# Kernel tuning notes

Measured on AMD Instinct MI355X. Metric: run time of the kernel, lower is better.

Reference implementation:

```python
import jax, jax.numpy as jnp
import numpy as np
from jax import lax

D_MODEL = 1024
D_INNER = 2048   # expand * d_model
D_STATE = 16
D_CONV = 4
DT_RANK = 64     # ceil(d_model / 16)
B_SZ, L_SEQ = 2, 2048


def setup_inputs() -> dict:
    key = jax.random.key(0)
    ks = jax.random.split(key, 12)
    s = lambda *sh: 1.0 / np.sqrt(sh[-1])
    inp = {
        "x": jax.random.normal(ks[0], (B_SZ, L_SEQ, D_MODEL), jnp.float32),
        "in_proj_w": jax.random.normal(ks[1], (2 * D_INNER, D_MODEL), jnp.float32) * s(D_MODEL),
        "conv_w": jax.random.normal(ks[2], (D_INNER, 1, D_CONV), jnp.float32) * 0.3,
        "conv_b": jax.random.normal(ks[3], (D_INNER,), jnp.float32) * 0.05,
        "x_proj_w": jax.random.normal(ks[4], (DT_RANK + 2 * D_STATE, D_INNER), jnp.float32) * s(D_INNER),
        "dt_proj_w": jax.random.normal(ks[5], (D_INNER, DT_RANK), jnp.float32) * s(DT_RANK),
        "dt_proj_b": jnp.log(jnp.exp(jax.random.uniform(ks[6], (D_INNER,), jnp.float32, 1e-3, 1e-1)) - 1.0),
        "A_log": jnp.log(jnp.broadcast_to(jnp.arange(1, D_STATE + 1, dtype=jnp.float32), (D_INNER, D_STATE))),
        "D": jnp.ones((D_INNER,), jnp.float32),
        "out_proj_w": jax.random.normal(ks[7], (D_MODEL, D_INNER), jnp.float32) * s(D_INNER),
        "ln_w": jnp.ones((D_MODEL,), jnp.float32),
        "ln_b": jnp.zeros((D_MODEL,), jnp.float32),
    }
    return inp


def _mamba(x, in_proj_w, conv_w, conv_b, x_proj_w, dt_proj_w, dt_proj_b, A_log, D, out_proj_w):
    # x: [B, L, d_model]
    xz = x @ in_proj_w.T                             # [B, L, 2*d_inner]
    u, z = jnp.split(xz, 2, axis=-1)                 # [B, L, d_inner] each
    # depthwise causal conv1d along L
    u_c = jnp.swapaxes(u, 1, 2)                      # [B, d_inner, L]
    u_c = lax.conv_general_dilated(
        u_c, conv_w, window_strides=(1,), padding=[(D_CONV - 1, 0)],
        feature_group_count=D_INNER, dimension_numbers=("NCH", "OIH", "NCH"))
    u_c = u_c + conv_b[None, :, None]
    u_c = jax.nn.silu(jnp.swapaxes(u_c, 1, 2))       # [B, L, d_inner]
    # input-dependent dt, B, C
    x_dbl = u_c @ x_proj_w.T                         # [B, L, dt_rank + 2*d_state]
    dt_lr = x_dbl[..., :DT_RANK]
    Bm = x_dbl[..., DT_RANK:DT_RANK + D_STATE]       # [B, L, d_state]
    Cm = x_dbl[..., DT_RANK + D_STATE:]              # [B, L, d_state]
    dt = jax.nn.softplus(dt_lr @ dt_proj_w.T + dt_proj_b)  # [B, L, d_inner]
    A = -jnp.exp(A_log)                              # [d_inner, d_state]

    def step(h, inputs):
        dt_t, b_t, c_t, u_t = inputs                 # [B,d_inner],[B,N],[B,N],[B,d_inner]
        dA = jnp.exp(dt_t[:, :, None] * A)           # [B, d_inner, N]
        h = h * dA + (dt_t * u_t)[:, :, None] * b_t[:, None, :]
        y_t = jnp.einsum("bdn,bn->bd", h, c_t)
        return h, y_t

    h0 = jnp.zeros((x.shape[0], D_INNER, D_STATE), x.dtype)
    xs = (jnp.swapaxes(dt, 0, 1), jnp.swapaxes(Bm, 0, 1),
          jnp.swapaxes(Cm, 0, 1), jnp.swapaxes(u_c, 0, 1))
    _, ys = lax.scan(step, h0, xs)                   # ys: [L, B, d_inner]
    y = jnp.swapaxes(ys, 0, 1) + u_c * D             # skip connection D*u
    y = y * jax.nn.silu(z)                           # gate
    return y @ out_proj_w.T                          # [B, L, d_model]


def _layernorm(x, w, b, eps=1e-5):
    mu = jnp.mean(x, axis=-1, keepdims=True)
    var = jnp.mean(jnp.square(x - mu), axis=-1, keepdims=True)
    return (x - mu) * lax.rsqrt(var + eps) * w + b


def reference(x, in_proj_w, conv_w, conv_b, x_proj_w, dt_proj_w, dt_proj_b,
              A_log, D, out_proj_w, ln_w, ln_b):
    y = _mamba(x, in_proj_w, conv_w, conv_b, x_proj_w, dt_proj_w, dt_proj_b,
               A_log, D, out_proj_w)
    return _layernorm(y + x, ln_w, ln_b)  # dropout_level=0 -> identity
```

## Files before the change

kernel.cpp:

```cpp
#include <hip/hip_runtime.h>
#include <hip/hip_bf16.h>
#include <math.h>

#define DEV static __device__ __forceinline__

typedef __hip_bfloat16 bf16;
typedef __attribute__((ext_vector_type(8))) short bf16x8;
typedef __attribute__((ext_vector_type(4))) short bf16x4;
typedef __attribute__((ext_vector_type(4))) float f32x4;

static constexpr int D_MODEL = 1024;
static constexpr int D_INNER = 2048;
static constexpr int D_STATE = 16;
static constexpr int DT_RANK = 64;
static constexpr int B_SZ   = 2;
static constexpr int L_SEQ  = 2048;
static constexpr int T_TOK  = B_SZ * L_SEQ;
static constexpr int LC     = 64;
static constexpr int NC     = L_SEQ / LC;
static constexpr int NXP    = DT_RANK + 2 * D_STATE;
static constexpr int KSPLIT = 8;

static constexpr int P_CONVW = 0;
static constexpr int P_CONVB = 8192;
static constexpr int P_DTB   = 10240;
static constexpr int P_ALOG  = 12288;
static constexpr int P_DW    = 45056;
static constexpr int P_LNW   = 47104;
static constexpr int P_LNB   = 48128;
static constexpr int P_TOT   = 49152;

DEV float bf2f(bf16 x) { return __bfloat162float(x); }
DEV bf16  f2bf(float x) { return __float2bfloat16(x); }
DEV float sigmoidf_(float x) { return 1.0f / (1.0f + __expf(-x)); }
DEV float s2f(short s) { bf16 b; __builtin_memcpy(&b, &s, 2); return bf2f(b); }
DEV short f2s(float x) { bf16 b = f2bf(x); short s; __builtin_memcpy(&s, &b, 2); return s; }

DEV bool probe_f32(const unsigned short* probe) { return probe[1] == 0; }

DEV void async_copy16(const void* g, void* l) {
  __builtin_amdgcn_global_load_lds(
      (const __attribute__((address_space(1))) void*)g,
      (__attribute__((address_space(3))) void*)l, 16, 0, 0);
}

template <int N>
DEV void vm_wait() {
  if constexpr (N == 8)      asm volatile("s_waitcnt vmcnt(8)" ::: "memory");
  else if constexpr (N == 6) asm volatile("s_waitcnt vmcnt(6)" ::: "memory");
  else                       asm volatile("s_waitcnt vmcnt(0)" ::: "memory");
}

__global__ void cvt_all(const void* s0, const void* s1, const void* s2,
                        const void* s3, const void* s4,
                        const void* s5, const void* s6, const void* s7,
                        const void* s8, const void* s9, const void* s10,
                        const void* s11,
                        bf16* d0, bf16* d1, bf16* d2, bf16* d3, bf16* d4,
                        float* params,
                        const unsigned short* __restrict__ probe)
{
  long i = (long)(blockIdx.x * 256 + threadIdx.x) * 4;
  const void* src; long off;
  bf16* dstb = nullptr; float* dstf = nullptr;
  if      (i <  4194304) { src = s0;  dstb = d0; off = i; }
  else if (i <  8388608) { src = s1;  dstb = d1; off = i - 4194304; }
  else if (i <  8585216) { src = s2;  dstb = d2; off = i - 8388608; }
  else if (i <  8716288) { src = s3;  dstb = d3; off = i - 8585216; }
  else if (i < 10813440) { src = s4;  dstb = d4; off = i - 8716288; }
  else if (i < 10821632) { src = s5;  dstf = params + P_CONVW; off = i - 10813440; }
  else if (i < 10823680) { src = s6;  dstf = params + P_CONVB; off = i - 10821632; }
  else if (i < 10825728) { src = s7;  dstf = params + P_DTB;   off = i - 10823680; }
  else if (i < 10858496) { src = s8;  dstf = params + P_ALOG;  off = i - 10825728; }
  else if (i < 10860544) { src = s9;  dstf = params + P_DW;    off = i - 10858496; }
  else if (i < 10861568) { src = s10; dstf = params + P_LNW;   off = i - 10860544; }
  else if (i < 10862592) { src = s11; dstf = params + P_LNB;   off = i - 10861568; }
  else return;
  bool isf32 = probe_f32(probe);
  float v[4];
  if (isf32) {
    float4 t = *(const float4*)((const float*)src + off);
    v[0] = t.x; v[1] = t.y; v[2] = t.z; v[3] = t.w;
  } else {
    short4 t = *(const short4*)((const bf16*)src + off);
    v[0] = s2f(t.x); v[1] = s2f(t.y); v[2] = s2f(t.z); v[3] = s2f(t.w);
  }
  if (dstb) {
    #pragma unroll
    for (int k = 0; k < 4; ++k) dstb[off + k] = f2bf(v[k]);
  } else {
    #pragma unroll
    for (int k = 0; k < 4; ++k) dstf[off + k] = v[k];
  }
}

DEV void stage256(const bf16* __restrict__ src, int ld, int base_row, int k0,
                  char* dst_base, int tid) {
  #pragma unroll
  for (int j = 0; j < 4; ++j) {
    int p   = j * 8192 + tid * 16;
    int row = p >> 7;
    int ck  = ((p >> 4) & 7) ^ (row & 7);
    async_copy16(src + (size_t)(base_row + row) * ld + k0 + ck * 8,
                 dst_base + j * 8192 + (tid >> 6) * 1024);
  }
}

template <int MODE>
DEV void gemm_pipe256(const bf16* __restrict__ A, const bf16* __restrict__ B,
                      int M, int K, int ld,
                      void* __restrict__ o0, void* __restrict__ o1)
{
  __shared__ __align__(16) char ring[2 * 65536];
  if (MODE == 3) {
    A += (size_t)blockIdx.z * K;
    B += (size_t)blockIdx.z * K;
  }
  const int tid  = threadIdx.x;
  const int wave = tid >> 6;
  const int lane = tid & 63;
  const int bm = blockIdx.x * 256;
  const int bn = blockIdx.y * 256;
  const int wmr = (wave >> 2) * 128;
  const int wnr = (wave & 3) * 64;
  const int fr = lane & 15;
  const int fq = lane >> 4;
  const int frs = lane & 7;
  const int NT = K / 64;

  f32x4 acc[8][4];
  #pragma unroll
  for (int i = 0; i < 8; ++i)
    #pragma unroll
    for (int j = 0; j < 4; ++j)
      #pragma unroll
      for (int r = 0; r < 4; ++r) acc[i][j][r] = 0.0f;

  stage256(A, ld, bm, 0,  ring,                 tid);
  stage256(B, ld, bn, 0,  ring + 32768,         tid);
  stage256(A, ld, bm, 64, ring + 65536,         tid);
  stage256(B, ld, bn, 64, ring + 65536 + 32768, tid);

  #pragma unroll 1
  for (int tk = 0; tk < NT; ++tk) {
    if (tk < NT - 1) vm_wait<8>();
    else             vm_wait<0>();
    __builtin_amdgcn_s_barrier();

    const char* sa = ring + (size_t)(tk & 1) * 65536;

    bf16x8 bg[4][2];
    #pragma unroll
    for (int ni = 0; ni < 4; ++ni)
      #pragma unroll
      for (int kk = 0; kk < 2; ++kk)
        bg[ni][kk] = *(const bf16x8*)(sa + 32768
                       + (size_t)(wnr + ni * 16 + fr) * 128
                       + (((kk * 4 + fq) ^ frs) * 16));

    __builtin_amdgcn_s_setprio(1);
    #pragma unroll
    for (int mh = 0; mh < 2; ++mh) {
      bf16x8 af[4][2];
      #pragma unroll
      for (int mi = 0; mi < 4; ++mi)
        #pragma unroll
        for (int kk = 0; kk < 2; ++kk)
          af[mi][kk] = *(const bf16x8*)(sa
                         + (size_t)(wmr + mh * 64 + mi * 16 + fr) * 128
                         + (((kk * 4 + fq) ^ frs) * 16));
      #pragma unroll
      for (int kk = 0; kk < 2; ++kk)
        #pragma unroll
        for (int mi = 0; mi < 4; ++mi)
          #pragma unroll
          for (int ni = 0; ni < 4; ++ni)
            acc[mh * 4 + mi][ni] = __builtin_amdgcn_mfma_f32_16x16x32_bf16(
                af[mi][kk], bg[ni][kk], acc[mh * 4 + mi][ni], 0, 0, 0);
    }
    __builtin_amdgcn_s_setprio(0);

    asm volatile("s_waitcnt lgkmcnt(0)" ::: "memory");
    __builtin_amdgcn_s_barrier();
    if (tk + 2 < NT) {
      char* sn = ring + (size_t)(tk & 1) * 65536;
      stage256(A, ld, bm, (tk + 2) * 64, sn,         tid);
      stage256(B, ld, bn, (tk + 2) * 64, sn + 32768, tid);
    }
  }

  const int er = (lane >> 4) * 4;
  const int ec = lane & 15;
  #pragma unroll
  for (int ai = 0; ai < 8; ++ai) {
    #pragma unroll
    for (int ni = 0; ni < 4; ++ni) {
      #pragma unroll
      for (int r = 0; r < 4; ++r) {
        int row = bm + wmr + ai * 16 + er + r;
        int col = bn + wnr + ni * 16 + ec;
        float v = acc[ai][ni][r];
        if (MODE == 0) {
          if (col < D_INNER) ((bf16*)o0)[(size_t)row * D_INNER + col] = f2bf(v);
          else               ((bf16*)o1)[(size_t)row * D_INNER + (col - D_INNER)] = f2bf(v * sigmoidf_(v));
        } else {
          int zz = blockIdx.z;
          bf16* dst = (zz < 2) ? (bf16*)o0 : (bf16*)o1;
          dst[(((size_t)(zz & 1)) * M + row) * D_MODEL + col] = f2bf(v);
        }
      }
    }
  }
}

template <int MODE>
DEV void gemm_body32(const bf16* __restrict__ A, const bf16* __restrict__ B,
                     int M, int N, int K, int ld,
                     void* __restrict__ o0, const void* __restrict__ e0)
{
  __shared__ __align__(16) bf16 As[128 * 32];
  __shared__ __align__(16) bf16 Bs[128 * 32];
  if (MODE == 1) {
    A += (size_t)blockIdx.z * K;
    B += (size_t)blockIdx.z * K;
  }
  const int tid  = threadIdx.x;
  const int wave = tid >> 6;
  const int lane = tid & 63;
  const int bm = blockIdx.x * 128;
  const int bn = blockIdx.y * 128;
  const int wm = (wave >> 1) * 64;
  const int wn = (wave & 1) * 64;

  f32x4 acc[4][4];
  #pragma unroll
  for (int i = 0; i < 4; ++i)
    #pragma unroll
    for (int j = 0; j < 4; ++j)
      #pragma unroll
      for (int r = 0; r < 4; ++r) acc[i][j][r] = 0.0f;

  const int ar0 = tid >> 2;
  const int ar1 = ar0 + 64;
  const int ac  = (tid & 3) * 8;
  const int fr = lane & 15;
  const int fk = (lane >> 4) * 8;

  for (int k0 = 0; k0 < K; k0 += 32) {
    bf16x8 a0 = *(const bf16x8*)(A + (size_t)(bm + ar0) * ld + k0 + ac);
    bf16x8 a1 = *(const bf16x8*)(A + (size_t)(bm + ar1) * ld + k0 + ac);
    int r0 = bn + ar0; if (r0 > N - 1) r0 = N - 1;
    int r1 = bn + ar1; if (r1 > N - 1) r1 = N - 1;
    bf16x8 b0 = *(const bf16x8*)(B + (size_t)r0 * ld + k0 + ac);
    bf16x8 b1 = *(const bf16x8*)(B + (size_t)r1 * ld + k0 + ac);
    __syncthreads();
    *(bf16x8*)(As + ar0 * 32 + ac) = a0;
    *(bf16x8*)(As + ar1 * 32 + ac) = a1;
    *(bf16x8*)(Bs + ar0 * 32 + ac) = b0;
    *(bf16x8*)(Bs + ar1 * 32 + ac) = b1;
    __syncthreads();

    bf16x8 af[4], bg[4];
    #pragma unroll
    for (int mi = 0; mi < 4; ++mi)
      af[mi] = *(const bf16x8*)(As + (wm + mi * 16 + fr) * 32 + fk);
    #pragma unroll
    for (int ni = 0; ni < 4; ++ni)
      bg[ni] = *(const bf16x8*)(Bs + (wn + ni * 16 + fr) * 32 + fk);
    #pragma unroll
    for (int mi = 0; mi < 4; ++mi)
      #pragma unroll
      for (int ni = 0; ni < 4; ++ni)
        acc[mi][ni] = __builtin_amdgcn_mfma_f32_16x16x32_bf16(af[mi], bg[ni], acc[mi][ni], 0, 0, 0);
  }

  const int er = (lane >> 4) * 4;
  const int ec = lane & 15;
  #pragma unroll
  for (int mi = 0; mi < 4; ++mi) {
    #pragma unroll
    for (int ni = 0; ni < 4; ++ni) {
      #pragma unroll
      for (int r = 0; r < 4; ++r) {
        int row = bm + wm + mi * 16 + er + r;
        int col = bn + wn + ni * 16 + ec;
        if (col >= N) continue;
        float v = acc[mi][ni][r];
        if (MODE == 1) {
          ((float*)o0)[((size_t)blockIdx.z * M + row) * N + col] = v;
        } else {
          v += ((const float*)e0)[col];
          float sp = (v > 15.0f) ? v : __logf(1.0f + __expf(v));
          ((bf16*)o0)[(size_t)row * D_INNER + col] = f2bf(sp);
        }
      }
    }
  }
}

__global__ void __launch_bounds__(512, 2) k_inproj(const bf16* A, const bf16* B,
    void* o0, void* o1) {
  gemm_pipe256<0>(A, B, T_TOK, D_MODEL, D_MODEL, o0, o1);
}
__global__ void __launch_bounds__(512, 2) k_outproj(const bf16* A, const bf16* B,
    void* o0, void* o1) {
  gemm_pipe256<3>(A, B, T_TOK, D_INNER / 4, D_INNER, o0, o1);
}
__global__ void __launch_bounds__(256) k_xproj(const bf16* A, const bf16* B,
    void* o0) {
  gemm_body32<1>(A, B, T_TOK, NXP, D_INNER / KSPLIT, D_INNER, o0, nullptr);
}
__global__ void __launch_bounds__(256) k_dtproj(const bf16* A, const bf16* B,
    void* o0, const void* e0) {
  gemm_body32<2>(A, B, T_TOK, D_INNER, DT_RANK, DT_RANK, o0, e0);
}

__global__ void xproj_post(const float* __restrict__ partials,
                           bf16* __restrict__ dtlr,
                           float* __restrict__ Bbuf,
                           float* __restrict__ Cbuf)
{
  int i = blockIdx.x * 256 + threadIdx.x;
  int col = i % NXP;
  int row = i / NXP;
  float s = 0.0f;
  #pragma unroll
  for (int kz = 0; kz < KSPLIT; ++kz)
    s += partials[((size_t)kz * T_TOK + row) * NXP + col];
  if      (col < DT_RANK)            dtlr[(size_t)row * DT_RANK + col] = f2bf(s);
  else if (col < DT_RANK + D_STATE)  Bbuf[(size_t)row * D_STATE + (col - DT_RANK)] = s;
  else                               Cbuf[(size_t)row * D_STATE + (col - DT_RANK - D_STATE)] = s;
}

__global__ void conv_silu_kernel(const bf16* __restrict__ u_pre,
                                 const float* __restrict__ cw,
                                 const float* __restrict__ cb,
                                 bf16* __restrict__ uc_bf)
{
  int idx = blockIdx.x * 256 + threadIdx.x;
  int d4 = (idx * 4) & (D_INNER - 1);
  int t  = (idx * 4) >> 11;
  int l  = t & (L_SEQ - 1);
  float4 bias = *(const float4*)(cb + d4);
  float acc[4] = {bias.x, bias.y, bias.z, bias.w};
  float4 wv[4];
  #pragma unroll
  for (int i = 0; i < 4; ++i) wv[i] = *(const float4*)(cw + (d4 + i) * 4);
  #pragma unroll
  for (int w = 0; w < 4; ++w) {
    if (l - 3 + w >= 0) {
      bf16x4 u = *(const bf16x4*)(u_pre + (size_t)(t - 3 + w) * D_INNER + d4);
      float uf[4];
      #pragma unroll
      for (int i = 0; i < 4; ++i) { short su = u[i]; uf[i] = s2f(su); }
      acc[0] += uf[0] * ((const float*)&wv[0])[w];
      acc[1] += uf[1] * ((const float*)&wv[1])[w];
      acc[2] += uf[2] * ((const float*)&wv[2])[w];
      acc[3] += uf[3] * ((const float*)&wv[3])[w];
    }
  }
  bf16x4 out;
  #pragma unroll
  for (int i = 0; i < 4; ++i) out[i] = f2s(acc[i] * sigmoidf_(acc[i]));
  *(bf16x4*)(uc_bf + (size_t)t * D_INNER + d4) = out;
}

DEV void load_Ad(const float* A_log, int d, float* Ad, bool& fast) {
  fast = true;
  #pragma unroll
  for (int n = 0; n < 16; ++n) {
    Ad[n] = -__expf(A_log[d * 16 + n]);
    fast = fast && (fabsf(Ad[n] + (float)(n + 1)) < 1e-3f * (n + 1));
  }
}
DEV void compute_decay(bool fast, float dtv, const float* Ad, float* dec) {
  if (fast) {
    float e1 = __expf(-dtv);
    float en = e1;
    #pragma unroll
    for (int n = 0; n < 16; ++n) { dec[n] = en; en *= e1; }
  } else {
    #pragma unroll
    for (int n = 0; n < 16; ++n) dec[n] = __expf(Ad[n] * dtv);
  }
}

__global__ __launch_bounds__(256) void scan_pass1(
    const bf16* __restrict__ dt, const bf16* __restrict__ uc_bf,
    const float* __restrict__ Bbuf, const float* __restrict__ A_log,
    float* __restrict__ hend, float* __restrict__ sumdt)
{
  __shared__ float Bs4[LC * D_STATE];
  __shared__ bf16 dts[16 * 256];
  __shared__ bf16 uts[16 * 256];
  int bid = blockIdx.x;
  int tid = threadIdx.x;
  int dt8 = bid & 7;
  int c = (bid >> 3) & (NC - 1);
  int b = bid >> 8;
  int d0 = dt8 * 256;
  int d  = d0 + tid;
  int t0g = b * L_SEQ + c * LC;

  ((f32x4*)Bs4)[tid] = ((const f32x4*)(Bbuf + (size_t)t0g * D_STATE))[tid];

  float Ad[16], h[16];
  bool fast;
  load_Ad(A_log, d, Ad, fast);
  #pragma unroll
  for (int n = 0; n < 16; ++n) h[n] = 0.0f;
  float sdt = 0.0f;

  for (int sub = 0; sub < 4; ++sub) {
    __syncthreads();
    #pragma unroll
    for (int rep = 0; rep < 2; ++rep) {
      int idx = rep * 256 + tid;
      int row = idx >> 5;
      int col = (idx & 31) * 8;
      size_t src = (size_t)(t0g + sub * 16 + row) * D_INNER + d0 + col;
      *(bf16x8*)(dts + row * 256 + col) = *(const bf16x8*)(dt + src);
      *(bf16x8*)(uts + row * 256 + col) = *(const bf16x8*)(uc_bf + src);
    }
    __syncthreads();
    for (int t = 0; t < 16; ++t) {
      float dtv = bf2f(dts[t * 256 + tid]);
      float uv  = bf2f(uts[t * 256 + tid]);
      float su  = dtv * uv;
      sdt += dtv;
      float dec[16];
      compute_decay(fast, dtv, Ad, dec);
      const float* Bp = Bs4 + (sub * 16 + t) * 16;
      #pragma unroll
      for (int n = 0; n < 16; ++n)
        h[n] = h[n] * dec[n] + su * Bp[n];
    }
  }
  size_t base = ((size_t)(b * NC + c) * D_INNER + d) * 16;
  #pragma unroll
  for (int q = 0; q < 4; ++q)
    *(f32x4*)(hend + base + q * 4) = *(f32x4*)(h + q * 4);
  sumdt[(size_t)(b * NC + c) * D_INNER + d] = sdt;
}

__global__ __launch_bounds__(256) void scan_pass2(
    float* __restrict__ hend, const float* __restrict__ sumdt,
    const float* __restrict__ A_log)
{
  __shared__ float Ms[4][64];
  __shared__ float Es[4][64];
  int bid = blockIdx.x;
  int tid = threadIdx.x;
  int cg   = tid >> 6;
  int lane = tid & 63;
  int dloc = lane >> 4;
  int n    = lane & 15;
  int b     = bid >> 9;
  int d     = (bid & 511) * 4 + dloc;

  float a = -__expf(A_log[d * 16 + n]);

  float Ml[8], El[8];
  float M = 1.0f, E = 0.0f;
  #pragma unroll
  for (int j = 0; j < 8; ++j) {
    int c = cg * 8 + j;
    size_t sbase = (size_t)(b * NC + c) * D_INNER + d;
    float m = __expf(a * sumdt[sbase]);
    float e = hend[sbase * 16 + n];
    Ml[j] = M; El[j] = E;
    M = m * M;
    E = m * E + e;
  }
  Ms[cg][lane] = M;
  Es[cg][lane] = E;
  __syncthreads();
  float Ep = 0.0f;
  for (int g = 0; g < cg; ++g) {
    float Mg = Ms[g][lane], Eg = Es[g][lane];
    Ep = Mg * Ep + Eg;
  }
  #pragma unroll
  for (int j = 0; j < 8; ++j) {
    int c = cg * 8 + j;
    size_t sbase = (size_t)(b * NC + c) * D_INNER + d;
    hend[sbase * 16 + n] = Ml[j] * Ep + El[j];
  }
}

__global__ __launch_bounds__(256) void scan_pass3(
    const bf16* __restrict__ dt, const bf16* __restrict__ uc_bf,
    const float* __restrict__ Bbuf, const float* __restrict__ Cbuf,
    const bf16* __restrict__ z_silu, const float* __restrict__ hstart,
    const float* __restrict__ A_log, const float* __restrict__ Dw,
    bf16* __restrict__ y_bf)
{
  __shared__ float Bs4[LC * D_STATE];
  __shared__ float Cs4[LC * D_STATE];
  __shared__ bf16 dts[16 * 256];
  __shared__ bf16 uts[16 * 256];
  __shared__ bf16 zts[16 * 256];
  int bid = blockIdx.x;
  int tid = threadIdx.x;
  int dt8 = bid & 7;
  int c = (bid >> 3) & (NC - 1);
  int b = bid >> 8;
  int d0 = dt8 * 256;
  int d  = d0 + tid;
  int t0g = b * L_SEQ + c * LC;

  ((f32x4*)Bs4)[tid] = ((const f32x4*)(Bbuf + (size_t)t0g * D_STATE))[tid];
  ((f32x4*)Cs4)[tid] = ((const f32x4*)(Cbuf + (size_t)t0g * D_STATE))[tid];

  float Ad[16], h[16];
  bool fast;
  load_Ad(A_log, d, Ad, fast);
  size_t base = ((size_t)(b * NC + c) * D_INNER + d) * 16;
  #pragma unroll
  for (int q = 0; q < 4; ++q)
    *(f32x4*)(h + q * 4) = *(const f32x4*)(hstart + base + q * 4);
  float Dv = Dw[d];

  for (int sub = 0; sub < 4; ++sub) {
    __syncthreads();
    #pragma unroll
    for (int rep = 0; rep < 2; ++rep) {
      int idx = rep * 256 + tid;
      int row = idx >> 5;
      int col = (idx & 31) * 8;
      size_t src = (size_t)(t0g + sub * 16 + row) * D_INNER + d0 + col;
      *(bf16x8*)(dts + row * 256 + col) = *(const bf16x8*)(dt + src);
      *(bf16x8*)(uts + row * 256 + col) = *(const bf16x8*)(uc_bf + src);
      *(bf16x8*)(zts + row * 256 + col) = *(const bf16x8*)(z_silu + src);
    }
    __syncthreads();
    for (int t = 0; t < 16; ++t) {
      float dtv = bf2f(dts[t * 256 + tid]);
      float uv  = bf2f(uts[t * 256 + tid]);
      float zv  = bf2f(zts[t * 256 + tid]);
      float su  = dtv * uv;
      float dec[16];
      compute_decay(fast, dtv, Ad, dec);
      const float* Bp = Bs4 + (sub * 16 + t) * 16;
      const float* Cp = Cs4 + (sub * 16 + t) * 16;
      float y = 0.0f;
      #pragma unroll
      for (int n = 0; n < 16; ++n) {
        h[n] = h[n] * dec[n] + su * Bp[n];
        y += h[n] * Cp[n];
      }
      y = (y + uv * Dv) * zv;
      y_bf[(size_t)(t0g + sub * 16 + t) * D_INNER + d] = f2bf(y);
    }
  }
}

__global__ void ln_kernel(const bf16* __restrict__ partsA,
                          const bf16* __restrict__ partsB,
                          const bf16* __restrict__ x_bf,
                          const float* __restrict__ w,
                          const float* __restrict__ bia,
                          void* __restrict__ out,
                          const unsigned short* __restrict__ probe)
{
  int t = blockIdx.x;
  int tid = threadIdx.x;
  const bf16* p0 = partsA + (size_t)t * D_MODEL;
  const bf16* p1 = partsA + ((size_t)T_TOK + t) * D_MODEL;
  const bf16* p2 = partsB + (size_t)t * D_MODEL;
  const bf16* p3 = partsB + ((size_t)T_TOK + t) * D_MODEL;
  const bf16* xr = x_bf + (size_t)t * D_MODEL;
  float v[4];
  float s = 0.0f, q = 0.0f;
  #pragma unroll
  for (int k = 0; k < 4; ++k) {
    int col = tid + k * 256;
    v[k] = bf2f(p0[col]) + bf2f(p1[col]) + bf2f(p2[col]) + bf2f(p3[col]) + bf2f(xr[col]);
    s += v[k]; q += v[k] * v[k];
  }
  #pragma unroll
  for (int off = 32; off >= 1; off >>= 1) {
    s += __shfl_down(s, off);
    q += __shfl_down(q, off);
  }
  __shared__ float red[8];
  __shared__ float mv[2];
  int wave = tid >> 6, lane = tid & 63;
  if (lane == 0) { red[wave] = s; red[4 + wave] = q; }
  __syncthreads();
  if (tid == 0) {
    float S = red[0] + red[1] + red[2] + red[3];
    float Q = red[4] + red[5] + red[6] + red[7];
    float mu = S * (1.0f / D_MODEL);
    float var = Q * (1.0f / D_MODEL) - mu * mu;
    mv[0] = mu; mv[1] = rsqrtf(var + 1e-5f);
  }
  __syncthreads();
  float mu = mv[0], rs = mv[1];
  bool isf32 = probe_f32(probe);
  #pragma unroll
  for (int k = 0; k < 4; ++k) {
    int col = tid + k * 256;
    float r = (v[k] - mu) * rs * w[col] + bia[col];
    if (isf32) ((float*)out)[(size_t)t * D_MODEL + col] = r;
    else       ((bf16*) out)[(size_t)t * D_MODEL + col] = f2bf(r);
  }
}

extern "C" void kernel_launch(void* const* d_in, const int* in_sizes, int n_in,
                              void* d_out, int out_size, void* d_ws, size_t ws_size,
                              hipStream_t stream)
{
  const void* x        = d_in[0];
  const void* in_w     = d_in[1];
  const void* conv_w   = d_in[2];
  const void* conv_b   = d_in[3];
  const void* xproj_w  = d_in[4];
  const void* dtproj_w = d_in[5];
  const void* dtproj_b = d_in[6];
  const void* A_log    = d_in[7];
  const void* Dw       = d_in[8];
  const void* out_w    = d_in[9];
  const void* ln_w     = d_in[10];
  const void* ln_b     = d_in[11];
  const unsigned short* probe = (const unsigned short*)A_log;

  char* p = (char*)d_ws;
  auto alloc = [&](size_t bytes) { char* r = p; p += (bytes + 255) & ~255ull; return r; };
  bf16*  x_bf   = (bf16*) alloc((size_t)T_TOK * D_MODEL * 2);
  bf16*  inw_bf = (bf16*) alloc((size_t)2 * D_INNER * D_MODEL * 2);
  bf16*  xpw_bf = (bf16*) alloc((size_t)NXP * D_INNER * 2);
  bf16*  dtw_bf = (bf16*) alloc((size_t)D_INNER * DT_RANK * 2);
  bf16*  outw_bf= (bf16*) alloc((size_t)D_MODEL * D_INNER * 2);
  float* params = (float*)alloc((size_t)P_TOT * 4);
  bf16*  u_pre  = (bf16*) alloc((size_t)T_TOK * D_INNER * 2);
  bf16*  z_silu = (bf16*) alloc((size_t)T_TOK * D_INNER * 2);
  bf16*  uc_bf  = (bf16*) alloc((size_t)T_TOK * D_INNER * 2);
  bf16*  dtlr   = (bf16*) alloc((size_t)T_TOK * DT_RANK * 2);
  float* Bbuf   = (float*)alloc((size_t)T_TOK * D_STATE * 4);
  float* Cbuf   = (float*)alloc((size_t)T_TOK * D_STATE * 4);
  bf16*  dtb    = (bf16*) alloc((size_t)T_TOK * D_INNER * 2);
  float* hend   = (float*)alloc((size_t)B_SZ * NC * D_INNER * 16 * 4);
  float* sumdt  = (float*)alloc((size_t)B_SZ * NC * D_INNER * 4);
  bf16*  y_bf   = u_pre;
  float* xparts = (float*)dtb;
  bf16*  opartsA = z_silu;
  bf16*  opartsB = dtb;

  dim3 blk(256);
  dim3 blk512(512);
  cvt_all<<<10608, blk, 0, stream>>>(x, in_w, xproj_w, dtproj_w, out_w,
                                     conv_w, conv_b, dtproj_b, A_log, Dw, ln_w, ln_b,
                                     x_bf, inw_bf, xpw_bf, dtw_bf, outw_bf, params, probe);

  k_inproj<<<dim3(T_TOK / 256, (2 * D_INNER) / 256), blk512, 0, stream>>>(x_bf, inw_bf, u_pre, z_silu);
  conv_silu_kernel<<<(T_TOK * D_INNER) / 1024, blk, 0, stream>>>(u_pre, params + P_CONVW, params + P_CONVB, uc_bf);
  k_xproj<<<dim3(T_TOK / 128, 1, KSPLIT), blk, 0, stream>>>(uc_bf, xpw_bf, xparts);
  xproj_post<<<(T_TOK * NXP) / 256, blk, 0, stream>>>(xparts, dtlr, Bbuf, Cbuf);
  k_dtproj<<<dim3(T_TOK / 128, D_INNER / 128), blk, 0, stream>>>(dtlr, dtw_bf, dtb, params + P_DTB);
  scan_pass1<<<B_SZ * NC * (D_INNER / 256), blk, 0, stream>>>(dtb, uc_bf, Bbuf, params + P_ALOG, hend, sumdt);
  scan_pass2<<<(B_SZ * D_INNER) / 2, blk, 0, stream>>>(hend, sumdt, params + P_ALOG);
  scan_pass3<<<B_SZ * NC * (D_INNER / 256), blk, 0, stream>>>(
      dtb, uc_bf, Bbuf, Cbuf, z_silu, hend, params + P_ALOG, params + P_DW, y_bf);
  k_outproj<<<dim3(T_TOK / 256, D_MODEL / 256, 4), blk512, 0, stream>>>(y_bf, outw_bf, opartsA, opartsB);
  ln_kernel<<<T_TOK, blk, 0, stream>>>(opartsA, opartsB, x_bf, params + P_LNW, params + P_LNB, d_out, probe);
}
```

Measured before the change: 305.2 us.

## Fuse x_proj reduction with dt_proj GEMM, vectorize convert, remap GEMM workgroups

Merges the split-K partial reduction of x_proj and the dt_proj GEMM with softplus into one kernel. It stages the reduced dt_lr tile in LDS and loops over all D_INNER column tiles, so the dtlr buffer round trip and one launch go away. The conversion kernel now moves 8 elements per thread with vector loads and stores. The 256-tile GEMMs remap the linear block id so neighbouring workgroups are spread across XCD-sized groups, aiming at better cache locality. The fused kernel launches only 32 blocks, each doing a serial loop of 16 tiles, so parallelism drops sharply for that stage.

New measurement: 409.2 us. 1.34x slower.

```diff
diff --git a/kernel.cpp b/kernel.cpp
--- a/kernel.cpp
+++ b/kernel.cpp
@@ -60,7 +60,7 @@
                         float* params,
                         const unsigned short* __restrict__ probe)
 {
-  long i = (long)(blockIdx.x * 256 + threadIdx.x) * 4;
+  long i = (long)(blockIdx.x * 256 + threadIdx.x) * 8;
   const void* src; long off;
   bf16* dstb = nullptr; float* dstf = nullptr;
   if      (i <  4194304) { src = s0;  dstb = d0; off = i; }
@@ -77,20 +77,27 @@
   else if (i < 10862592) { src = s11; dstf = params + P_LNB;   off = i - 10861568; }
   else return;
   bool isf32 = probe_f32(probe);
-  float v[4];
+  float v[8];
   if (isf32) {
-    float4 t = *(const float4*)((const float*)src + off);
-    v[0] = t.x; v[1] = t.y; v[2] = t.z; v[3] = t.w;
+    float4 a = *(const float4*)((const float*)src + off);
+    float4 b = *(const float4*)((const float*)src + off + 4);
+    v[0]=a.x; v[1]=a.y; v[2]=a.z; v[3]=a.w;
+    v[4]=b.x; v[5]=b.y; v[6]=b.z; v[7]=b.w;
   } else {
-    short4 t = *(const short4*)((const bf16*)src + off);
-    v[0] = s2f(t.x); v[1] = s2f(t.y); v[2] = s2f(t.z); v[3] = s2f(t.w);
+    bf16x8 t = *(const bf16x8*)((const bf16*)src + off);
+    #pragma unroll
+    for (int k = 0; k < 8; ++k) { short sk = t[k]; v[k] = s2f(sk); }
   }
   if (dstb) {
-    #pragma unroll
-    for (int k = 0; k < 4; ++k) dstb[off + k] = f2bf(v[k]);
+    bf16x8 o;
+    #pragma unroll
+    for (int k = 0; k < 8; ++k) o[k] = f2s(v[k]);
+    *(bf16x8*)(dstb + off) = o;
   } else {
-    #pragma unroll
-    for (int k = 0; k < 4; ++k) dstf[off + k] = v[k];
+    f32x4 a = {v[0], v[1], v[2], v[3]};
+    f32x4 b = {v[4], v[5], v[6], v[7]};
+    *(f32x4*)(dstf + off)     = a;
+    *(f32x4*)(dstf + off + 4) = b;
   }
 }
 
@@ -112,15 +119,25 @@
                       void* __restrict__ o0, void* __restrict__ o1)
 {
   __shared__ __align__(16) char ring[2 * 65536];
+
+  unsigned lin = blockIdx.x + gridDim.x * (blockIdx.y + gridDim.y * blockIdx.z);
+  unsigned nwg = gridDim.x * gridDim.y * gridDim.z;
+  unsigned cpx = nwg >> 3;
+  unsigned nid = (lin & 7) * cpx + (lin >> 3);
+  unsigned bx  = nid % gridDim.x;
+  unsigned tq  = nid / gridDim.x;
+  unsigned by  = tq % gridDim.y;
+  unsigned bz  = tq / gridDim.y;
+
   if (MODE == 3) {
-    A += (size_t)blockIdx.z * K;
-    B += (size_t)blockIdx.z * K;
+    A += (size_t)bz * K;
+    B += (size_t)bz * K;
   }
   const int tid  = threadIdx.x;
   const int wave = tid >> 6;
   const int lane = tid & 63;
-  const int bm = blockIdx.x * 256;
-  const int bn = blockIdx.y * 256;
+  const int bm = bx * 256;
+  const int bn = by * 256;
   const int wmr = (wave >> 2) * 128;
   const int wnr = (wave & 3) * 64;
   const int fr = lane & 15;
@@ -204,9 +221,8 @@
           if (col < D_INNER) ((bf16*)o0)[(size_t)row * D_INNER + col] = f2bf(v);
           else               ((bf16*)o1)[(size_t)row * D_INNER + (col - D_INNER)] = f2bf(v * sigmoidf_(v));
         } else {
-          int zz = blockIdx.z;
-          bf16* dst = (zz < 2) ? (bf16*)o0 : (bf16*)o1;
-          dst[(((size_t)(zz & 1)) * M + row) * D_MODEL + col] = f2bf(v);
+          bf16* dst = (bz < 2) ? (bf16*)o0 : (bf16*)o1;
+          dst[(((size_t)(bz & 1)) * M + row) * D_MODEL + col] = f2bf(v);
         }
       }
     }
@@ -286,13 +302,7 @@
         int col = bn + wn + ni * 16 + ec;
         if (col >= N) continue;
         float v = acc[mi][ni][r];
-        if (MODE == 1) {
-          ((float*)o0)[((size_t)blockIdx.z * M + row) * N + col] = v;
-        } else {
-          v += ((const float*)e0)[col];
-          float sp = (v > 15.0f) ? v : __logf(1.0f + __expf(v));
-          ((bf16*)o0)[(size_t)row * D_INNER + col] = f2bf(sp);
-        }
+        ((float*)o0)[((size_t)blockIdx.z * M + row) * N + col] = v;
       }
     }
   }
@@ -310,26 +320,100 @@
     void* o0) {
   gemm_body32<1>(A, B, T_TOK, NXP, D_INNER / KSPLIT, D_INNER, o0, nullptr);
 }
-__global__ void __launch_bounds__(256) k_dtproj(const bf16* A, const bf16* B,
-    void* o0, const void* e0) {
-  gemm_body32<2>(A, B, T_TOK, D_INNER, DT_RANK, DT_RANK, o0, e0);
-}
-
-__global__ void xproj_post(const float* __restrict__ partials,
-                           bf16* __restrict__ dtlr,
-                           float* __restrict__ Bbuf,
-                           float* __restrict__ Cbuf)
-{
-  int i = blockIdx.x * 256 + threadIdx.x;
-  int col = i % NXP;
-  int row = i / NXP;
-  float s = 0.0f;
-  #pragma unroll
-  for (int kz = 0; kz < KSPLIT; ++kz)
-    s += partials[((size_t)kz * T_TOK + row) * NXP + col];
-  if      (col < DT_RANK)            dtlr[(size_t)row * DT_RANK + col] = f2bf(s);
-  else if (col < DT_RANK + D_STATE)  Bbuf[(size_t)row * D_STATE + (col - DT_RANK)] = s;
-  else                               Cbuf[(size_t)row * D_STATE + (col - DT_RANK - D_STATE)] = s;
+
+__global__ __launch_bounds__(256) void k_dtfuse(
+    const float* __restrict__ partials,
+    const bf16*  __restrict__ dtw,
+    const float* __restrict__ dtbias,
+    float* __restrict__ Bbuf, float* __restrict__ Cbuf,
+    bf16* __restrict__ dtb)
+{
+  __shared__ __align__(16) bf16 Al[128 * 72];
+  __shared__ __align__(16) bf16 Bl[128 * 72];
+  const int tid = threadIdx.x;
+  const int r0  = blockIdx.x * 128;
+
+  #pragma unroll
+  for (int it = 0; it < 12; ++it) {
+    int idx = it * 256 + tid;
+    int row = idx / 24;
+    int g   = idx - row * 24;
+    f32x4 s = {0.0f, 0.0f, 0.0f, 0.0f};
+    #pragma unroll
+    for (int kz = 0; kz < KSPLIT; ++kz)
+      s += *(const f32x4*)(partials + ((size_t)kz * T_TOK + r0 + row) * NXP + g * 4);
+    if (g < 16) {
+      bf16x4 o;
+      #pragma unroll
+      for (int k = 0; k < 4; ++k) o[k] = f2s(s[k]);
+      *(bf16x4*)(Al + row * 72 + g * 4) = o;
+    } else if (g < 20) {
+      *(f32x4*)(Bbuf + (size_t)(r0 + row) * D_STATE + (g - 16) * 4) = s;
+    } else {
+      *(f32x4*)(Cbuf + (size_t)(r0 + row) * D_STATE + (g - 20) * 4) = s;
+    }
+  }
+  __syncthreads();
+
+  const int wave = tid >> 6;
+  const int lane = tid & 63;
+  const int wm = (wave >> 1) * 64;
+  const int wn = (wave & 1) * 64;
+  const int fr = lane & 15;
+  const int fk = (lane >> 4) * 8;
+  const int er = (lane >> 4) * 4;
+  const int ec = lane & 15;
+
+  for (int bn = 0; bn < D_INNER; bn += 128) {
+    #pragma unroll
+    for (int it = 0; it < 4; ++it) {
+      int idx = it * 256 + tid;
+      int row = idx >> 3;
+      int cv  = (idx & 7) * 8;
+      *(bf16x8*)(Bl + row * 72 + cv) = *(const bf16x8*)(dtw + (size_t)(bn + row) * 64 + cv);
+    }
+    __syncthreads();
+
+    f32x4 acc[4][4];
+    #pragma unroll
+    for (int i = 0; i < 4; ++i)
+      #pragma unroll
+      for (int j = 0; j < 4; ++j)
+        #pragma unroll
+        for (int r = 0; r < 4; ++r) acc[i][j][r] = 0.0f;
+
+    #pragma unroll
+    for (int k0 = 0; k0 < 64; k0 += 32) {
+      bf16x8 af[4], bg[4];
+      #pragma unroll
+      for (int mi = 0; mi < 4; ++mi)
+        af[mi] = *(const bf16x8*)(Al + (wm + mi * 16 + fr) * 72 + k0 + fk);
+      #pragma unroll
+      for (int ni = 0; ni < 4; ++ni)
+        bg[ni] = *(const bf16x8*)(Bl + (wn + ni * 16 + fr) * 72 + k0 + fk);
+      #pragma unroll
+      for (int mi = 0; mi < 4; ++mi)
+        #pragma unroll
+        for (int ni = 0; ni < 4; ++ni)
+          acc[mi][ni] = __builtin_amdgcn_mfma_f32_16x16x32_bf16(af[mi], bg[ni], acc[mi][ni], 0, 0, 0);
+    }
+
+    #pragma unroll
+    for (int mi = 0; mi < 4; ++mi) {
+      #pragma unroll
+      for (int ni = 0; ni < 4; ++ni) {
+        #pragma unroll
+        for (int r = 0; r < 4; ++r) {
+          int orow = r0 + wm + mi * 16 + er + r;
+          int ocol = bn + wn + ni * 16 + ec;
+          float v = acc[mi][ni][r] + dtbias[ocol];
+          float sp = (v > 15.0f) ? v : __logf(1.0f + __expf(v));
+          dtb[(size_t)orow * D_INNER + ocol] = f2bf(sp);
+        }
+      }
+    }
+    __syncthreads();
+  }
 }
 
 __global__ void conv_silu_kernel(const bf16* __restrict__ u_pre,
@@ -642,22 +726,22 @@
   bf16*  dtb    = (bf16*) alloc((size_t)T_TOK * D_INNER * 2);
   float* hend   = (float*)alloc((size_t)B_SZ * NC * D_INNER * 16 * 4);
   float* sumdt  = (float*)alloc((size_t)B_SZ * NC * D_INNER * 4);
+  (void)dtlr;
   bf16*  y_bf   = u_pre;
-  float* xparts = (float*)dtb;
+  float* xparts = (float*)u_pre;
   bf16*  opartsA = z_silu;
   bf16*  opartsB = dtb;
 
   dim3 blk(256);
   dim3 blk512(512);
-  cvt_all<<<10608, blk, 0, stream>>>(x, in_w, xproj_w, dtproj_w, out_w,
-                                     conv_w, conv_b, dtproj_b, A_log, Dw, ln_w, ln_b,
-                                     x_bf, inw_bf, xpw_bf, dtw_bf, outw_bf, params, probe);
+  cvt_all<<<5304, blk, 0, stream>>>(x, in_w, xproj_w, dtproj_w, out_w,
+                                    conv_w, conv_b, dtproj_b, A_log, Dw, ln_w, ln_b,
+                                    x_bf, inw_bf, xpw_bf, dtw_bf, outw_bf, params, probe);
 
   k_inproj<<<dim3(T_TOK / 256, (2 * D_INNER) / 256), blk512, 0, stream>>>(x_bf, inw_bf, u_pre, z_silu);
   conv_silu_kernel<<<(T_TOK * D_INNER) / 1024, blk, 0, stream>>>(u_pre, params + P_CONVW, params + P_CONVB, uc_bf);
   k_xproj<<<dim3(T_TOK / 128, 1, KSPLIT), blk, 0, stream>>>(uc_bf, xpw_bf, xparts);
-  xproj_post<<<(T_TOK * NXP) / 256, blk, 0, stream>>>(xparts, dtlr, Bbuf, Cbuf);
-  k_dtproj<<<dim3(T_TOK / 128, D_INNER / 128), blk, 0, stream>>>(dtlr, dtw_bf, dtb, params + P_DTB);
+  k_dtfuse<<<T_TOK / 128, blk, 0, stream>>>(xparts, dtw_bf, params + P_DTB, Bbuf, Cbuf, dtb);
   scan_pass1<<<B_SZ * NC * (D_INNER / 256), blk, 0, stream>>>(dtb, uc_bf, Bbuf, params + P_ALOG, hend, sumdt);
   scan_pass2<<<(B_SZ * D_INNER) / 2, blk, 0, stream>>>(hend, sumdt, params + P_ALOG);
   scan_pass3<<<B_SZ * NC * (D_INNER / 256), blk, 0, stream>>>(
```
